# Kernel optimization log

Measured on AMD Instinct MI355X. Metric: run time of the kernel, lower is better.

## Reference

```python
import jax, jax.numpy as jnp
import numpy as np

B, D_MODEL, D_MEM, H, N_MEM = 128, 1024, 64, 16, 4096


def setup_inputs() -> dict:
    key = jax.random.key(0)
    ks = jax.random.split(key, 6)
    scale = 1.0 / np.sqrt(D_MODEL)
    return {
        "query": jax.random.normal(ks[0], (B, D_MODEL), jnp.float32),
        "addresses": jax.random.normal(ks[1], (N_MEM, D_MEM), jnp.float32),
        "memories": jax.random.normal(ks[2], (B, N_MEM, D_MEM), jnp.float32),
        "Wq": jax.random.normal(ks[3], (D_MODEL, D_MODEL), jnp.float32) * scale,
        "bq": jnp.zeros((D_MODEL,), jnp.float32),
        "Wm": jax.random.normal(ks[4], (D_MODEL, D_MODEL), jnp.float32) * scale,
        "bm": jnp.zeros((D_MODEL,), jnp.float32),
    }


def reference(query, addresses, memories, Wq, bq, Wm, bm):
    # query projection -> heads: (B, H, d_mem)
    q = (query @ Wq.T + bq).reshape(B, H, D_MEM)
    # stage 1: build linear-attention kernel over the memory-slot dim
    k = jax.nn.relu(memories + addresses)            # (B, N, d_mem)
    matrix = jnp.einsum('bnd,bne->bde', k, memories)  # (B, d_mem, d_mem)
    normalizer = jnp.sum(k, axis=-2)                  # (B, d_mem)
    # stage 2: read the kernel with activated queries
    qa = jax.nn.relu(q)                               # (B, H, d_mem)
    numerator = jnp.einsum('bhd,bde->bhe', qa, matrix)
    denominator = jnp.einsum('bhd,bd->bh', qa, normalizer)[..., None] + 1e-5
    attn = numerator / denominator                    # (B, H, d_mem)
    return attn.reshape(B, H * D_MEM) @ Wm.T + bm     # (B, d_model)
```

## Files before the change

kernel.cpp:

```cpp
#include <hip/hip_runtime.h>
#include <hip/hip_bf16.h>

#define BATCH 128
#define DMEM 64
#define NMEM 4096
#define DMODEL 1024
#define S1 4
#define LDS_STRIDE 40

typedef __bf16 v8bf __attribute__((ext_vector_type(8)));
typedef __bf16 v2bf __attribute__((ext_vector_type(2)));
typedef float v4f __attribute__((ext_vector_type(4)));
typedef float v16f __attribute__((ext_vector_type(16)));

__device__ __forceinline__ void gemm_sk(const float* __restrict__ A,
                                        const float* __restrict__ W,
                                        float* __restrict__ dst,
                                        int m0, int n0, int k0,
                                        float* smem) {
    float(*As)[36] = (float(*)[36])smem;
    float(*Ws)[36] = (float(*)[36])(smem + 32 * 36);
    const int t = threadIdx.x;
    const int lrow = t >> 3;
    const int lc4 = (t & 7) * 4;
    const int rp = t >> 4;
    const int cp = t & 15;

    float acc00 = 0.f, acc01 = 0.f, acc10 = 0.f, acc11 = 0.f;

    v4f av = *(const v4f*)&A[(size_t)(m0 + lrow) * DMODEL + k0 + lc4];
    v4f wv = *(const v4f*)&W[(size_t)(n0 + lrow) * DMODEL + k0 + lc4];

    for (int c = 0; c < 4; ++c) {
        __syncthreads();
        *(v4f*)&As[lrow][lc4] = av;
        *(v4f*)&Ws[lrow][lc4] = wv;
        __syncthreads();
        if (c + 1 < 4) {
            const int kc = k0 + (c + 1) * 32;
            av = *(const v4f*)&A[(size_t)(m0 + lrow) * DMODEL + kc + lc4];
            wv = *(const v4f*)&W[(size_t)(n0 + lrow) * DMODEL + kc + lc4];
        }
#pragma unroll
        for (int kk = 0; kk < 32; kk += 4) {
            v4f a0 = *(v4f*)&As[rp][kk];
            v4f a1 = *(v4f*)&As[rp + 16][kk];
            v4f b0 = *(v4f*)&Ws[cp][kk];
            v4f b1 = *(v4f*)&Ws[cp + 16][kk];
#pragma unroll
            for (int q = 0; q < 4; ++q) {
                acc00 = fmaf(a0[q], b0[q], acc00);
                acc01 = fmaf(a0[q], b1[q], acc01);
                acc10 = fmaf(a1[q], b0[q], acc10);
                acc11 = fmaf(a1[q], b1[q], acc11);
            }
        }
    }
    dst[(size_t)(m0 + rp) * DMODEL + n0 + cp] = acc00;
    dst[(size_t)(m0 + rp) * DMODEL + n0 + cp + 16] = acc01;
    dst[(size_t)(m0 + rp + 16) * DMODEL + n0 + cp] = acc10;
    dst[(size_t)(m0 + rp + 16) * DMODEL + n0 + cp + 16] = acc11;
}

__global__ __launch_bounds__(256, 3) void k1(const float* __restrict__ mem,
                                             const float* __restrict__ addr,
                                             float* __restrict__ pmat,
                                             float* __restrict__ pnorm,
                                             const float* __restrict__ query,
                                             const float* __restrict__ Wq,
                                             float* __restrict__ qa_p) {
    __shared__ __align__(16) char smem[24576];
    const int bid = blockIdx.x;
    const int nst = BATCH * S1;

    if (bid >= nst) {
        const int b2 = bid - nst;
        const int m0 = (b2 & 3) * 32;
        const int n0 = ((b2 >> 2) & 31) * 32;
        const int ks = b2 >> 7;
        gemm_sk(query, Wq, qa_p + (size_t)ks * BATCH * DMODEL,
                m0, n0, ks * 128, (float*)smem);
        return;
    }

    float* norm_s = (float*)(smem + 20480);

    const int t = threadIdx.x;
    const int b = bid & (BATCH - 1);
    const int s = bid >> 7;
    const int slots_per = NMEM / S1;
    const int chunks = slots_per >> 5;

    const int u = t & 15;
    const int v = t >> 4;
    const int d0 = u * 4;

    const int l = t & 63;
    const int wv = t >> 6;
    const int strip = wv >> 1;
    const int kh = wv & 1;
    const int lrow = l & 31;
    const int lh = l >> 5;

    const size_t mem_base = ((size_t)b * NMEM + (size_t)s * slots_per) * DMEM;
    const size_t addr_base = (size_t)s * slots_per * DMEM;
    const size_t so = (size_t)(2 * v) * DMEM + d0;

    v16f acc0, acc1;
#pragma unroll
    for (int r = 0; r < 16; ++r) { acc0[r] = 0.f; acc1[r] = 0.f; }
    float nacc[4] = {0.f, 0.f, 0.f, 0.f};

    v4f mE0 = *(const v4f*)&mem[mem_base + so];
    v4f mE1 = *(const v4f*)&mem[mem_base + so + DMEM];
    v4f aE0 = *(const v4f*)&addr[addr_base + so];
    v4f aE1 = *(const v4f*)&addr[addr_base + so + DMEM];
    v4f mO0 = *(const v4f*)&mem[mem_base + 2048 + so];
    v4f mO1 = *(const v4f*)&mem[mem_base + 2048 + so + DMEM];
    v4f aO0 = *(const v4f*)&addr[addr_base + 2048 + so];
    v4f aO1 = *(const v4f*)&addr[addr_base + 2048 + so + DMEM];

    __bf16* kb0 = (__bf16*)smem;
    __bf16* mb0 = kb0 + 64 * LDS_STRIDE;
    __bf16* kb1 = (__bf16*)(smem + 10240);
    __bf16* mb1 = kb1 + 64 * LDS_STRIDE;
    const int cb = 16 * kh + 8 * lh;

    for (int cc = 0; cc < chunks; cc += 2) {
#pragma unroll
        for (int i = 0; i < 4; ++i) {
            float kf0 = fmaxf(mE0[i] + aE0[i], 0.f);
            float kf1 = fmaxf(mE1[i] + aE1[i], 0.f);
            nacc[i] += kf0 + kf1;
            v2bf kp; kp[0] = (__bf16)kf0; kp[1] = (__bf16)kf1;
            v2bf mp; mp[0] = (__bf16)mE0[i]; mp[1] = (__bf16)mE1[i];
            *(v2bf*)&kb0[(d0 + i) * LDS_STRIDE + 2 * v] = kp;
            *(v2bf*)&mb0[(d0 + i) * LDS_STRIDE + 2 * v] = mp;
        }
        if (cc + 2 < chunks) {
            const size_t coff = (size_t)(cc + 2) * 32 * DMEM;
            mE0 = *(const v4f*)&mem[mem_base + coff + so];
            mE1 = *(const v4f*)&mem[mem_base + coff + so + DMEM];
            aE0 = *(const v4f*)&addr[addr_base + coff + so];
            aE1 = *(const v4f*)&addr[addr_base + coff + so + DMEM];
        }
        __syncthreads();
        {
            v8bf af = *(v8bf*)&kb0[(32 * strip + lrow) * LDS_STRIDE + cb];
            v8bf b0 = *(v8bf*)&mb0[lrow * LDS_STRIDE + cb];
            v8bf b1 = *(v8bf*)&mb0[(32 + lrow) * LDS_STRIDE + cb];
            acc0 = __builtin_amdgcn_mfma_f32_32x32x16_bf16(af, b0, acc0, 0, 0, 0);
            acc1 = __builtin_amdgcn_mfma_f32_32x32x16_bf16(af, b1, acc1, 0, 0, 0);
        }
#pragma unroll
        for (int i = 0; i < 4; ++i) {
            float kf0 = fmaxf(mO0[i] + aO0[i], 0.f);
            float kf1 = fmaxf(mO1[i] + aO1[i], 0.f);
            nacc[i] += kf0 + kf1;
            v2bf kp; kp[0] = (__bf16)kf0; kp[1] = (__bf16)kf1;
            v2bf mp; mp[0] = (__bf16)mO0[i]; mp[1] = (__bf16)mO1[i];
            *(v2bf*)&kb1[(d0 + i) * LDS_STRIDE + 2 * v] = kp;
            *(v2bf*)&mb1[(d0 + i) * LDS_STRIDE + 2 * v] = mp;
        }
        if (cc + 3 < chunks) {
            const size_t coff = (size_t)(cc + 3) * 32 * DMEM;
            mO0 = *(const v4f*)&mem[mem_base + coff + so];
            mO1 = *(const v4f*)&mem[mem_base + coff + so + DMEM];
            aO0 = *(const v4f*)&addr[addr_base + coff + so];
            aO1 = *(const v4f*)&addr[addr_base + coff + so + DMEM];
        }
        __syncthreads();
        {
            v8bf af = *(v8bf*)&kb1[(32 * strip + lrow) * LDS_STRIDE + cb];
            v8bf b0 = *(v8bf*)&mb1[lrow * LDS_STRIDE + cb];
            v8bf b1 = *(v8bf*)&mb1[(32 + lrow) * LDS_STRIDE + cb];
            acc0 = __builtin_amdgcn_mfma_f32_32x32x16_bf16(af, b0, acc0, 0, 0, 0);
            acc1 = __builtin_amdgcn_mfma_f32_32x32x16_bf16(af, b1, acc1, 0, 0, 0);
        }
    }

    __syncthreads();
    float* red = (float*)smem;
#pragma unroll
    for (int i = 0; i < 4; ++i) norm_s[v * 64 + d0 + i] = nacc[i];
    if (kh == 1) {
#pragma unroll
        for (int r = 0; r < 16; ++r) {
            int row = (r & 3) + 8 * (r >> 2) + 4 * lh;
            int d = 32 * strip + row;
            red[lrow * 68 + d] = acc0[r];
            red[(32 + lrow) * 68 + d] = acc1[r];
        }
    }
    __syncthreads();
    if (kh == 0) {
#pragma unroll
        for (int r = 0; r < 16; ++r) {
            int row = (r & 3) + 8 * (r >> 2) + 4 * lh;
            int d = 32 * strip + row;
            red[lrow * 68 + d] += acc0[r];
            red[(32 + lrow) * 68 + d] += acc1[r];
        }
    }
    __syncthreads();
    {
        float* pm = pmat + ((size_t)s * BATCH + b) * 4096;
        const int e = t >> 2;
        const int ds = (t & 3) * 16;
#pragma unroll
        for (int j = 0; j < 4; ++j)
            *(v4f*)&pm[e * 64 + ds + 4 * j] = *(v4f*)&red[e * 68 + ds + 4 * j];
    }
    if (t < 64) {
        float ssum = 0.f;
#pragma unroll
        for (int g = 0; g < 16; ++g) ssum += norm_s[g * 64 + t];
        pnorm[((size_t)s * BATCH + b) * 64 + t] = ssum;
    }
}

__global__ __launch_bounds__(256) void stage2(const float* __restrict__ pmat,
                                              const float* __restrict__ pnorm,
                                              const float* __restrict__ qa_p,
                                              const float* __restrict__ bq,
                                              float* __restrict__ attn) {
    __shared__ float mat_s[16 * 68];
    __shared__ float qa_s[16 * 68];
    __shared__ float nrm_s[64];
    const int t = threadIdx.x;
    const int b = blockIdx.x >> 2;
    const int eq = blockIdx.x & 3;

    {
        const int i4 = t * 4;
        v4f acc = (v4f){0.f, 0.f, 0.f, 0.f};
#pragma unroll
        for (int s = 0; s < S1; ++s)
            acc += *(const v4f*)&pmat[((size_t)s * BATCH + b) * 4096 + eq * 1024 + i4];
        *(v4f*)&mat_s[(i4 >> 6) * 68 + (i4 & 63)] = acc;
    }
#pragma unroll
    for (int i = 0; i < 4; ++i) {
        const int idx = t + 256 * i;
        float ssum = 0.f;
#pragma unroll
        for (int ks = 0; ks < 8; ++ks)
            ssum += qa_p[((size_t)ks * BATCH + b) * DMODEL + idx];
        qa_s[(idx >> 6) * 68 + (idx & 63)] = fmaxf(ssum + bq[idx], 0.f);
    }
    if (t < 64) {
        float ssum = 0.f;
#pragma unroll
        for (int s = 0; s < S1; ++s)
            ssum += pnorm[((size_t)s * BATCH + b) * 64 + t];
        nrm_s[t] = ssum;
    }
    __syncthreads();

    const int h = t >> 4;
    const int e = t & 15;
    float num = 0.f, den = 0.f;
#pragma unroll 8
    for (int d = 0; d < 64; ++d) {
        float q = qa_s[h * 68 + d];
        num = fmaf(q, mat_s[e * 68 + d], num);
        den = fmaf(q, nrm_s[d], den);
    }
    attn[(size_t)b * DMODEL + h * 64 + eq * 16 + e] = num / (den + 1e-5f);
}

__global__ __launch_bounds__(256) void gemm_out(const float* __restrict__ A,
                                                const float* __restrict__ W,
                                                float* __restrict__ out_p) {
    __shared__ __align__(16) float smem[2 * 32 * 36];
    const int ks = blockIdx.z;
    gemm_sk(A, W, out_p + (size_t)ks * BATCH * DMODEL,
            blockIdx.x * 32, blockIdx.y * 32, ks * 128, smem);
}

__global__ __launch_bounds__(256) void combine(const float* __restrict__ out_p,
                                               const float* __restrict__ bm,
                                               float* __restrict__ out) {
    const int i = blockIdx.x * 256 + threadIdx.x;
    float ssum = bm[i & (DMODEL - 1)];
#pragma unroll
    for (int ks = 0; ks < 8; ++ks)
        ssum += out_p[(size_t)ks * BATCH * DMODEL + i];
    out[i] = ssum;
}

extern "C" void kernel_launch(void* const* d_in, const int* in_sizes, int n_in,
                              void* d_out, int out_size, void* d_ws, size_t ws_size,
                              hipStream_t stream) {
    const float* query     = (const float*)d_in[0];
    const float* addresses = (const float*)d_in[1];
    const float* memories  = (const float*)d_in[2];
    const float* Wq        = (const float*)d_in[3];
    const float* bq        = (const float*)d_in[4];
    const float* Wm        = (const float*)d_in[5];
    const float* bm        = (const float*)d_in[6];
    float* out = (float*)d_out;
    float* ws = (float*)d_ws;

    float* qa_p    = ws;
    float* attn_ws = qa_p + 1048576;
    float* pnorm   = attn_ws + 131072;
    float* pmat    = pnorm + 32768;
    float* out_p   = pmat + 2097152;

    k1<<<dim3(BATCH * S1 + 1024), 256, 0, stream>>>(memories, addresses, pmat,
                                                    pnorm, query, Wq, qa_p);
    stage2<<<dim3(512), 256, 0, stream>>>(pmat, pnorm, qa_p, bq, attn_ws);
    gemm_out<<<dim3(4, 32, 8), 256, 0, stream>>>(attn_ws, Wm, out_p);
    combine<<<dim3(512), 256, 0, stream>>>(out_p, bm, out);
}
```

Measured before the change: 226.5 us.

## Enlarge GEMM tiles to 64x64 and fuse split-K reduction via atomics

Both projection GEMMs now use 64x64 output tiles, with each thread computing a 4x4 block instead of 2x2. This raises register-level reuse and cuts the GEMM block count fourfold. The output GEMM drops its partial-sum buffer and separate combine kernel. It atomically adds split-K partials straight into the output, which stage2 pre-initialises with the bias. This saves one launch and the partial-buffer traffic, at the cost of atomic contention, non-deterministic summation order, and fewer blocks for the GPU to spread across its compute units.

```diff
diff --git a/kernel.cpp b/kernel.cpp
--- a/kernel.cpp
+++ b/kernel.cpp
@@ -13,53 +13,71 @@
 typedef float v4f __attribute__((ext_vector_type(4)));
 typedef float v16f __attribute__((ext_vector_type(16)));
 
-__device__ __forceinline__ void gemm_sk(const float* __restrict__ A,
-                                        const float* __restrict__ W,
-                                        float* __restrict__ dst,
-                                        int m0, int n0, int k0,
-                                        float* smem) {
+template <int ATOMIC>
+__device__ __forceinline__ void gemm64(const float* __restrict__ A,
+                                       const float* __restrict__ W,
+                                       float* __restrict__ dst,
+                                       int m0, int n0, int k0,
+                                       float* smem) {
     float(*As)[36] = (float(*)[36])smem;
-    float(*Ws)[36] = (float(*)[36])(smem + 32 * 36);
+    float(*Ws)[36] = (float(*)[36])(smem + 64 * 36);
     const int t = threadIdx.x;
-    const int lrow = t >> 3;
-    const int lc4 = (t & 7) * 4;
+    const int lrow = t >> 2;
+    const int lc8 = (t & 3) * 8;
     const int rp = t >> 4;
     const int cp = t & 15;
 
-    float acc00 = 0.f, acc01 = 0.f, acc10 = 0.f, acc11 = 0.f;
-
-    v4f av = *(const v4f*)&A[(size_t)(m0 + lrow) * DMODEL + k0 + lc4];
-    v4f wv = *(const v4f*)&W[(size_t)(n0 + lrow) * DMODEL + k0 + lc4];
+    float acc[4][4];
+#pragma unroll
+    for (int j = 0; j < 4; ++j)
+#pragma unroll
+        for (int i = 0; i < 4; ++i) acc[j][i] = 0.f;
+
+    v4f av0 = *(const v4f*)&A[(size_t)(m0 + lrow) * DMODEL + k0 + lc8];
+    v4f av1 = *(const v4f*)&A[(size_t)(m0 + lrow) * DMODEL + k0 + lc8 + 4];
+    v4f wv0 = *(const v4f*)&W[(size_t)(n0 + lrow) * DMODEL + k0 + lc8];
+    v4f wv1 = *(const v4f*)&W[(size_t)(n0 + lrow) * DMODEL + k0 + lc8 + 4];
 
     for (int c = 0; c < 4; ++c) {
         __syncthreads();
-        *(v4f*)&As[lrow][lc4] = av;
-        *(v4f*)&Ws[lrow][lc4] = wv;
+        *(v4f*)&As[lrow][lc8] = av0;
+        *(v4f*)&As[lrow][lc8 + 4] = av1;
+        *(v4f*)&Ws[lrow][lc8] = wv0;
+        *(v4f*)&Ws[lrow][lc8 + 4] = wv1;
         __syncthreads();
         if (c + 1 < 4) {
             const int kc = k0 + (c + 1) * 32;
-            av = *(const v4f*)&A[(size_t)(m0 + lrow) * DMODEL + kc + lc4];
-            wv = *(const v4f*)&W[(size_t)(n0 + lrow) * DMODEL + kc + lc4];
+            av0 = *(const v4f*)&A[(size_t)(m0 + lrow) * DMODEL + kc + lc8];
+            av1 = *(const v4f*)&A[(size_t)(m0 + lrow) * DMODEL + kc + lc8 + 4];
+            wv0 = *(const v4f*)&W[(size_t)(n0 + lrow) * DMODEL + kc + lc8];
+            wv1 = *(const v4f*)&W[(size_t)(n0 + lrow) * DMODEL + kc + lc8 + 4];
         }
 #pragma unroll
         for (int kk = 0; kk < 32; kk += 4) {
-            v4f a0 = *(v4f*)&As[rp][kk];
-            v4f a1 = *(v4f*)&As[rp + 16][kk];
-            v4f b0 = *(v4f*)&Ws[cp][kk];
-            v4f b1 = *(v4f*)&Ws[cp + 16][kk];
-#pragma unroll
-            for (int q = 0; q < 4; ++q) {
-                acc00 = fmaf(a0[q], b0[q], acc00);
-                acc01 = fmaf(a0[q], b1[q], acc01);
-                acc10 = fmaf(a1[q], b0[q], acc10);
-                acc11 = fmaf(a1[q], b1[q], acc11);
-            }
-        }
-    }
-    dst[(size_t)(m0 + rp) * DMODEL + n0 + cp] = acc00;
-    dst[(size_t)(m0 + rp) * DMODEL + n0 + cp + 16] = acc01;
-    dst[(size_t)(m0 + rp + 16) * DMODEL + n0 + cp] = acc10;
-    dst[(size_t)(m0 + rp + 16) * DMODEL + n0 + cp + 16] = acc11;
+            v4f a[4], b[4];
+#pragma unroll
+            for (int j = 0; j < 4; ++j) a[j] = *(v4f*)&As[rp + 16 * j][kk];
+#pragma unroll
+            for (int i = 0; i < 4; ++i) b[i] = *(v4f*)&Ws[cp + 16 * i][kk];
+#pragma unroll
+            for (int j = 0; j < 4; ++j)
+#pragma unroll
+                for (int i = 0; i < 4; ++i)
+#pragma unroll
+                    for (int q = 0; q < 4; ++q)
+                        acc[j][i] = fmaf(a[j][q], b[i][q], acc[j][i]);
+        }
+    }
+#pragma unroll
+    for (int j = 0; j < 4; ++j)
+#pragma unroll
+        for (int i = 0; i < 4; ++i) {
+            float* p = &dst[(size_t)(m0 + rp + 16 * j) * DMODEL + n0 + cp + 16 * i];
+            if (ATOMIC)
+                unsafeAtomicAdd(p, acc[j][i]);
+            else
+                *p = acc[j][i];
+        }
 }
 
 __global__ __launch_bounds__(256, 3) void k1(const float* __restrict__ mem,
@@ -75,11 +93,11 @@
 
     if (bid >= nst) {
         const int b2 = bid - nst;
-        const int m0 = (b2 & 3) * 32;
-        const int n0 = ((b2 >> 2) & 31) * 32;
-        const int ks = b2 >> 7;
-        gemm_sk(query, Wq, qa_p + (size_t)ks * BATCH * DMODEL,
-                m0, n0, ks * 128, (float*)smem);
+        const int m0 = (b2 & 1) * 64;
+        const int n0 = ((b2 >> 1) & 15) * 64;
+        const int ks = b2 >> 5;
+        gemm64<0>(query, Wq, qa_p + (size_t)ks * BATCH * DMODEL,
+                  m0, n0, ks * 128, (float*)smem);
         return;
     }
 
@@ -223,13 +241,17 @@
                                               const float* __restrict__ pnorm,
                                               const float* __restrict__ qa_p,
                                               const float* __restrict__ bq,
-                                              float* __restrict__ attn) {
+                                              float* __restrict__ attn,
+                                              const float* __restrict__ bm,
+                                              float* __restrict__ out) {
     __shared__ float mat_s[16 * 68];
     __shared__ float qa_s[16 * 68];
     __shared__ float nrm_s[64];
     const int t = threadIdx.x;
     const int b = blockIdx.x >> 2;
     const int eq = blockIdx.x & 3;
+
+    out[(size_t)b * DMODEL + eq * 256 + t] = bm[eq * 256 + t];
 
     {
         const int i4 = t * 4;
@@ -271,22 +293,10 @@
 
 __global__ __launch_bounds__(256) void gemm_out(const float* __restrict__ A,
                                                 const float* __restrict__ W,
-                                                float* __restrict__ out_p) {
-    __shared__ __align__(16) float smem[2 * 32 * 36];
-    const int ks = blockIdx.z;
-    gemm_sk(A, W, out_p + (size_t)ks * BATCH * DMODEL,
-            blockIdx.x * 32, blockIdx.y * 32, ks * 128, smem);
-}
-
-__global__ __launch_bounds__(256) void combine(const float* __restrict__ out_p,
-                                               const float* __restrict__ bm,
-                                               float* __restrict__ out) {
-    const int i = blockIdx.x * 256 + threadIdx.x;
-    float ssum = bm[i & (DMODEL - 1)];
-#pragma unroll
-    for (int ks = 0; ks < 8; ++ks)
-        ssum += out_p[(size_t)ks * BATCH * DMODEL + i];
-    out[i] = ssum;
+                                                float* __restrict__ out) {
+    __shared__ __align__(16) float smem[2 * 64 * 36];
+    gemm64<1>(A, W, out, blockIdx.x * 64, blockIdx.y * 64, blockIdx.z * 128,
+              smem);
 }
 
 extern "C" void kernel_launch(void* const* d_in, const int* in_sizes, int n_in,
@@ -306,11 +316,9 @@
     float* attn_ws = qa_p + 1048576;
     float* pnorm   = attn_ws + 131072;
     float* pmat    = pnorm + 32768;
-    float* out_p   = pmat + 2097152;
-
-    k1<<<dim3(BATCH * S1 + 1024), 256, 0, stream>>>(memories, addresses, pmat,
-                                                    pnorm, query, Wq, qa_p);
-    stage2<<<dim3(512), 256, 0, stream>>>(pmat, pnorm, qa_p, bq, attn_ws);
-    gemm_out<<<dim3(4, 32, 8), 256, 0, stream>>>(attn_ws, Wm, out_p);
-    combine<<<dim3(512), 256, 0, stream>>>(out_p, bm, out);
-}
+
+    k1<<<dim3(BATCH * S1 + 256), 256, 0, stream>>>(memories, addresses, pmat,
+                                                   pnorm, query, Wq, qa_p);
+    stage2<<<dim3(512), 256, 0, stream>>>(pmat, pnorm, qa_p, bq, attn_ws, bm, out);
+    gemm_out<<<dim3(2, 16, 8), 256, 0, stream>>>(attn_ws, Wm, out);
+}
```

Result: no change. 227.5 us (+0.5%).
